# Kernel optimization log

Measured on AMD Instinct MI355X. Metric: run time of the kernel, lower is better.

The kernel has to match this reference:

```python
import jax, jax.numpy as jnp
import numpy as np

EMBED_DIM = 1024
NUM_HEADS = 16
HEAD_DIM = EMBED_DIM // NUM_HEADS
SCALING = HEAD_DIM ** -0.5
NEG_FILL = -1e30


def setup_inputs() -> dict:
    key = jax.random.key(0)
    k1, k2, k3 = jax.random.split(key, 3)
    T, B, E = 2048, 4, EMBED_DIM
    query = jax.random.normal(k1, (T, B, E), dtype=jnp.float32)
    key_padding_mask = jnp.zeros((B, T), dtype=bool)  # 1 = padded key
    # xavier_uniform-like init
    lim_in = (6.0 / (3 * E + E)) ** 0.5
    in_proj_weight = jax.random.uniform(k2, (3 * E, E), minval=-lim_in, maxval=lim_in, dtype=jnp.float32)
    in_proj_bias = jnp.zeros((3 * E,), dtype=jnp.float32)
    lim_out = (6.0 / (E + E)) ** 0.5
    out_w = jax.random.uniform(k3, (E, E), minval=-lim_out, maxval=lim_out, dtype=jnp.float32)
    out_b = jnp.zeros((E,), dtype=jnp.float32)
    return {"query": query, "key_padding_mask": key_padding_mask,
            "in_proj_weight": in_proj_weight, "in_proj_bias": in_proj_bias,
            "out_w": out_w, "out_b": out_b}


def reference(query, key_padding_mask, in_proj_weight, in_proj_bias, out_w, out_b):
    T, B, E = query.shape
    H, D = NUM_HEADS, HEAD_DIM
    # fused in-projection (self-attention: qkv from same input)
    qkv = query @ in_proj_weight.T + in_proj_bias  # [T,B,3E]
    q, k, v = jnp.split(qkv, 3, axis=-1)
    q = q * SCALING
    q = q.reshape(T, B, H, D)
    k = k.reshape(T, B, H, D)
    v = v.reshape(T, B, H, D)
    # attention scores [B,H,T,S]
    scores = jnp.einsum('tbhd,sbhd->bhts', q, k)
    scores = jnp.where(key_padding_mask[:, None, None, :], NEG_FILL, scores)
    attn_w = jax.nn.softmax(scores, axis=-1)  # [B,H,T,S]
    # weighted sum of values -> [T,B,E]
    attn = jnp.einsum('bhts,sbhd->tbhd', attn_w, v).reshape(T, B, E)
    attn = attn @ out_w.T + out_b
    attn_w_avg = jnp.sum(attn_w, axis=1) / H  # [B,T,S]
    return attn, attn_w_avg
```

## Files before the change

### kernel.cpp

```cpp
#include <hip/hip_runtime.h>
#include <stdint.h>

#define QSCALE 0.18033688011112042f

typedef unsigned short u16;
typedef unsigned int u32;
typedef unsigned long long u64;
typedef _Float16 f16;
typedef __attribute__((ext_vector_type(2))) __fp16 h16x2;
typedef __attribute__((ext_vector_type(8))) _Float16 f16x8;
typedef __attribute__((ext_vector_type(8))) __bf16 bf16x8;
typedef __attribute__((ext_vector_type(4))) float f32x4;
typedef __attribute__((ext_vector_type(16))) float f32x16;
typedef __attribute__((ext_vector_type(8))) u16 u16x8;
typedef __attribute__((ext_vector_type(4))) u32 u32x4;

__device__ __forceinline__ void gl_lds16(const void* g, void* l) {
  __builtin_amdgcn_global_load_lds(
      (const __attribute__((address_space(1))) void*)g,
      (__attribute__((address_space(3))) void*)l, 16, 0, 0);
}

__device__ __forceinline__ u16 f2bf(float f) {
  unsigned int u = __float_as_uint(f);
  u += 0x7FFFu + ((u >> 16) & 1u);
  return (u16)(u >> 16);
}

extern "C" __global__ __launch_bounds__(256) void cvt_all(
    const float* __restrict__ query, const float* __restrict__ w_in,
    const float* __restrict__ w_out, u16* __restrict__ dst) {
  int i = (blockIdx.x * 256 + threadIdx.x) * 4;
  const float* src;
  int off;
  if (i < 8388608) {
    src = query; off = i;
  } else if (i < 11534336) {
    src = w_in; off = i - 8388608;
  } else {
    src = w_out; off = i - 11534336;
  }
  float4 v = *(const float4*)(src + off);
  ushort4 o;
  o.x = f2bf(v.x); o.y = f2bf(v.y); o.z = f2bf(v.z); o.w = f2bf(v.w);
  *(ushort4*)(dst + i) = o;
}

extern "C" __global__ __launch_bounds__(128) void mask_bits(
    const unsigned char* __restrict__ mask, u64* __restrict__ mbits) {
  const int i = threadIdx.x;
  const unsigned char* p = mask + i * 64;
  u64 bits = 0;
#pragma unroll
  for (int j = 0; j < 8; ++j) {
    const u64 c = *(const u64*)(p + j * 8);
#pragma unroll
    for (int bb = 0; bb < 8; ++bb)
      if ((c >> (8 * bb)) & 0xFFull) bits |= 1ull << (j * 8 + bb);
  }
  mbits[i] = bits;
}

extern "C" __global__ __launch_bounds__(256) void gemm_qkv(
    const u16* __restrict__ X, const u16* __restrict__ W,
    const float* __restrict__ bias,
    u16* __restrict__ qb, u16* __restrict__ kb, u16* __restrict__ vtb) {
  const int tid = threadIdx.x;
  const int w = tid >> 6, lane = tid & 63;
  const int lg = lane >> 4, ll = lane & 15;
  const int wm = w >> 1, wn = w & 1;

  const int xcd = blockIdx.x & 7;
  const int i6 = blockIdx.x >> 3;
  const int tx = xcd * 8 + (i6 & 7);
  const int ty = i6 >> 3;
  const int row0A = tx * 128;
  const int row0B = ty * 128;

  __shared__ __align__(16) u16 SM[16384];
  u16* Asb = SM;
  u16* Bsb = SM + 8192;

  f32x4 acc[4][4] = {};

  const int r_st = tid >> 2;
  const int cb_st = (tid & 3) * 16;

#pragma unroll
  for (int it = 0; it < 2; ++it) {
    gl_lds16((const char*)X + ((size_t)(row0A + it * 64 + r_st) * 1024) * 2 + cb_st,
             (char*)Asb + it * 4096 + w * 1024);
    gl_lds16((const char*)W + ((size_t)(row0B + it * 64 + r_st) * 1024) * 2 + cb_st,
             (char*)Bsb + it * 4096 + w * 1024);
  }

  for (int kt = 0; kt < 32; ++kt) {
    const int cur = kt & 1;
    asm volatile("s_waitcnt vmcnt(0)" ::: "memory");
    __syncthreads();
    if (kt + 1 < 32) {
      const int k0 = (kt + 1) * 32;
      const int nxt = cur ^ 1;
#pragma unroll
      for (int it = 0; it < 2; ++it) {
        gl_lds16((const char*)X + ((size_t)(row0A + it * 64 + r_st) * 1024 + k0) * 2 + cb_st,
                 (char*)(Asb + nxt * 4096) + it * 4096 + w * 1024);
        gl_lds16((const char*)W + ((size_t)(row0B + it * 64 + r_st) * 1024 + k0) * 2 + cb_st,
                 (char*)(Bsb + nxt * 4096) + it * 4096 + w * 1024);
      }
    }
    const u16* Ab = Asb + cur * 4096;
    const u16* Bb = Bsb + cur * 4096;
    const int kc = lg * 8;
    bf16x8 a[4], bfr[4];
#pragma unroll
    for (int i = 0; i < 4; ++i)
      a[i] = *(const bf16x8*)(Ab + (wm * 64 + i * 16 + ll) * 32 + kc);
#pragma unroll
    for (int j = 0; j < 4; ++j)
      bfr[j] = *(const bf16x8*)(Bb + (wn * 64 + j * 16 + ll) * 32 + kc);
#pragma unroll
    for (int i = 0; i < 4; ++i)
#pragma unroll
      for (int j = 0; j < 4; ++j)
        acc[i][j] = __builtin_amdgcn_mfma_f32_16x16x32_bf16(a[i], bfr[j], acc[i][j], 0, 0, 0);
  }

  __syncthreads();
  const int which = row0B >> 10;
  const float scl = which == 0 ? QSCALE : 1.0f;
  const int hh0 = (row0B & 1023) >> 6;

#pragma unroll
  for (int j = 0; j < 4; ++j) {
    const int n = row0B + wn * 64 + j * 16 + ll;
    const float bv = bias[n];
#pragma unroll
    for (int i = 0; i < 4; ++i)
#pragma unroll
      for (int r = 0; r < 4; ++r) {
        const float val = (acc[i][j][r] + bv) * scl;
        u16 pay;
        if (which == 2) {
          const f16 hv = (f16)val;
          pay = __builtin_bit_cast(u16, hv);
        } else {
          pay = f2bf(val);
        }
        const int lrow = wn * 128 + r * 32 + wm * 16 + i * 4 + lg;
        const int slot = (j * 2 + (ll >> 3)) ^ (lrow & 7);
        SM[lrow * 64 + slot * 8 + (ll & 7)] = pay;
      }
  }
  __syncthreads();

  if (which < 2) {
    u16* dst = which ? kb : qb;
    const int lrow = tid;
    const int hh = hh0 + (lrow >> 7);
    const int bb = (lrow >> 5) & 3;
    const int tt = (row0A >> 2) + (lrow & 31);
    u16* gp = dst + ((size_t)(bb * 16 + hh) * 2048 + tt) * 64;
#pragma unroll
    for (int s = 0; s < 8; ++s)
      *(u16x8*)(gp + s * 8) = *(const u16x8*)(SM + lrow * 64 + ((s ^ (lrow & 7)) << 3));
  } else {
#pragma unroll
    for (int u = 0; u < 2; ++u) {
      const int rid = u * 256 + tid;
      const int bb = rid >> 7, hhr = (rid >> 6) & 1, dd = rid & 63;
      const int hh = hh0 + hhr;
      const int slot0 = dd >> 3, de = dd & 7;
      u16 col[32];
#pragma unroll
      for (int t2 = 0; t2 < 32; ++t2) {
        const int lrow = hhr * 128 + bb * 32 + t2;
        col[t2] = SM[lrow * 64 + ((slot0 ^ (lrow & 7)) << 3) + de];
      }
      u16* gp = vtb + ((size_t)(bb * 16 + hh) * 64 + dd) * 2048 + (row0A >> 2);
#pragma unroll
      for (int sg = 0; sg < 4; ++sg)
        *(u16x8*)(gp + sg * 8) = *(const u16x8*)(col + sg * 8);
    }
  }
}

extern "C" __global__ __launch_bounds__(256, 4) void flash_fwd(
    const u16* __restrict__ q, const u16* __restrict__ k,
    const u16* __restrict__ vt, const u64* __restrict__ mbits,
    u16* __restrict__ attn_pre, float* __restrict__ stat_il) {
  const int lb = ((blockIdx.x & 7) << 7) + (blockIdx.x >> 3);
  const int bh = lb >> 4, tt = lb & 15;
  const int b = bh >> 4, hd = bh & 15;
  const int t0 = tt * 128;
  const int tid = threadIdx.x, w = tid >> 6, lane = tid & 63;
  const int hl = lane >> 5;
  const int l31 = lane & 31;

  __shared__ __align__(16) u16 Ks[2][64 * 64];
  __shared__ __align__(16) u16 Vs[2][64 * 64];

  const int qrow = t0 + w * 32 + l31;
  const u16* qp = q + ((size_t)bh * 2048 + qrow) * 64 + hl * 8;
  bf16x8 qreg[4];
#pragma unroll
  for (int kg = 0; kg < 4; ++kg) qreg[kg] = *(const bf16x8*)(qp + kg * 16);

  f32x16 po[2] = {};
  float ls0 = 0.f, ls1 = 0.f;
  const h16x2 ones = {(__fp16)1.0f, (__fp16)1.0f};

  const int slot_r = tid >> 3;
  const int slot_c8 = (tid & 7) ^ (slot_r & 7);

#define STAGE_F(buf, s0_)                                                      \
  do {                                                                         \
    _Pragma("unroll") for (int it2 = 0; it2 < 2; ++it2) {                      \
      const int rr = it2 * 32 + slot_r;                                        \
      gl_lds16((const char*)k +                                                \
                   (((size_t)bh * 2048 + (s0_) + rr) * 64 + slot_c8 * 8) * 2,  \
               (char*)&Ks[buf][0] + it2 * 4096 + w * 1024);                    \
      gl_lds16((const char*)vt +                                               \
                   (((size_t)bh * 64 + rr) * 2048 + (s0_) + slot_c8 * 8) * 2,  \
               (char*)&Vs[buf][0] + it2 * 4096 + w * 1024);                    \
    }                                                                          \
  } while (0)

  STAGE_F(0, 0);
  asm volatile("s_waitcnt vmcnt(0)" ::: "memory");
  __builtin_amdgcn_s_barrier();

  for (int t = 0; t < 32; ++t) {
    const u64 mb = mbits[b * 32 + t];
    const int cur = t & 1;
    if (t + 1 < 32) STAGE_F(cur ^ 1, (t + 1) * 64);

    const char* Kb = (const char*)&Ks[cur][0];
    const char* Vb = (const char*)&Vs[cur][0];

#pragma unroll
    for (int kt = 0; kt < 2; ++kt) {
      f32x16 z = {};
      const int key = kt * 32 + l31;
      __builtin_amdgcn_s_setprio(1);
#pragma unroll
      for (int kg = 0; kg < 4; ++kg) {
        const bf16x8 kf = *(const bf16x8*)(
            Kb + key * 128 + ((((kg << 1) | hl) ^ (key & 7)) << 4));
        z = __builtin_amdgcn_mfma_f32_32x32x16_bf16(kf, qreg[kg], z, 0, 0, 0);
      }
      __builtin_amdgcn_s_setprio(0);

      float ps[16];
#pragma unroll
      for (int r = 0; r < 16; ++r) ps[r] = __builtin_amdgcn_exp2f(z[r]);
      const u32 m32 = (u32)(mb >> (kt * 32));
      if (m32) {
#pragma unroll
        for (int r = 0; r < 16; ++r) {
          const int bitpos = (r & 3) + 8 * (r >> 2) + 4 * hl;
          if ((m32 >> bitpos) & 1u) ps[r] = 0.f;
        }
      }

      u32 w8[8];
#pragma unroll
      for (int j = 0; j < 8; ++j) {
        const h16x2 pk = __builtin_amdgcn_cvt_pkrtz(ps[2 * j], ps[2 * j + 1]);
        w8[j] = __builtin_bit_cast(u32, pk);
        if (j & 1)
          ls1 = __builtin_amdgcn_fdot2(pk, ones, ls1, false);
        else
          ls0 = __builtin_amdgcn_fdot2(pk, ones, ls0, false);
      }

#pragma unroll
      for (int f = 0; f < 2; ++f) {
        u32 d0 = w8[4 * f], d1 = w8[4 * f + 1];
        u32 s0w = w8[4 * f + 2], s1w = w8[4 * f + 3];
        asm volatile("v_permlane32_swap_b32 %0, %1" : "+v"(d0), "+v"(s0w));
        asm volatile("v_permlane32_swap_b32 %0, %1" : "+v"(d1), "+v"(s1w));
        const f16x8 pa = __builtin_bit_cast(f16x8, (u32x4){d0, d1, s0w, s1w});
        const int g = kt * 2 + f;
        __builtin_amdgcn_s_setprio(1);
#pragma unroll
        for (int dt = 0; dt < 2; ++dt) {
          const int d = dt * 32 + l31;
          const f16x8 vf = *(const f16x8*)(
              Vb + d * 128 + ((((g << 1) | hl) ^ (d & 7)) << 4));
          po[dt] = __builtin_amdgcn_mfma_f32_32x32x16_f16(pa, vf, po[dt], 0, 0, 0);
        }
        __builtin_amdgcn_s_setprio(0);
      }
    }

    asm volatile("s_waitcnt vmcnt(0)" ::: "memory");
    __builtin_amdgcn_s_barrier();
  }

  float lsum = ls0 + ls1;
  lsum += __shfl_xor(lsum, 32, 64);
  const float linv = 1.0f / lsum;
  if (lane < 32)
    stat_il[(size_t)bh * 2048 + t0 + w * 32 + lane] = linv;

#pragma unroll
  for (int r = 0; r < 16; ++r) {
    const int qi = (r & 3) + 8 * (r >> 2) + 4 * hl;
    const float lv = __shfl(linv, qi, 64);
    const int trow = t0 + w * 32 + qi;
#pragma unroll
    for (int dt = 0; dt < 2; ++dt) {
      const int dd = dt * 32 + l31;
      attn_pre[((size_t)(trow * 4 + b)) * 1024 + hd * 64 + dd] =
          f2bf(po[dt][r] * lv);
    }
  }
#undef STAGE_F
}

extern "C" __global__ __launch_bounds__(256, 3) void wavg(
    const u16* __restrict__ q, const u16* __restrict__ k,
    const u64* __restrict__ mbits,
    const float* __restrict__ stat_il, float* __restrict__ wout) {
  const int lb = ((blockIdx.x & 7) << 8) + (blockIdx.x >> 3);
  const int b = lb >> 9, tt = (lb >> 5) & 15, st = lb & 31;
  const int t0 = tt * 128, s0 = st * 64;
  const int tid = threadIdx.x, w = tid >> 6, lane = tid & 63;
  const int hl = lane >> 5;
  const int l31 = lane & 31;

  __shared__ __align__(16) u16 Qs[2][128 * 64];
  __shared__ __align__(16) u16 Ks2[2][64 * 64];

  const int slot_r8 = tid >> 3;
  const int slot_c8 = (tid & 7) ^ (slot_r8 & 7);

  const u64 mbw = mbits[b * 32 + st];
  const u32 m32lo = (u32)mbw, m32hi = (u32)(mbw >> 32);
  const bool domask = mbw != 0ull;

#define STAGE_W(buf, hh)                                                       \
  do {                                                                         \
    const size_t qo_ = (size_t)(b * 16 + (hh)) * 2048;                         \
    _Pragma("unroll") for (int i2 = 0; i2 < 4; ++i2) {                         \
      const int rr = i2 * 32 + slot_r8;                                        \
      gl_lds16((const char*)q + ((qo_ + t0 + rr) * 64 + slot_c8 * 8) * 2,      \
               (char*)&Qs[buf][0] + i2 * 4096 + w * 1024);                     \
    }                                                                          \
    _Pragma("unroll") for (int i2 = 0; i2 < 2; ++i2) {                         \
      const int rr = i2 * 32 + slot_r8;                                        \
      gl_lds16((const char*)k + ((qo_ + s0 + rr) * 64 + slot_c8 * 8) * 2,      \
               (char*)&Ks2[buf][0] + i2 * 4096 + w * 1024);                    \
    }                                                                          \
  } while (0)

  STAGE_W(0, 0);
  asm volatile("s_waitcnt vmcnt(0)" ::: "memory");
  __syncthreads();

  float accw[32] = {};
  for (int h = 0; h < 16; ++h) {
    const int cur = h & 1;
    const float ilh =
        stat_il[(size_t)(b * 16 + h) * 2048 + t0 + w * 32 + l31];

    if (h + 1 < 16) STAGE_W(cur ^ 1, h + 1);

    const char* Qb = (const char*)&Qs[cur][0];
    const char* Kb = (const char*)&Ks2[cur][0];

    const int qr = w * 32 + l31;
    bf16x8 qf[4];
#pragma unroll
    for (int kg = 0; kg < 4; ++kg)
      qf[kg] = *(const bf16x8*)(
          Qb + qr * 128 + ((((kg << 1) | hl) ^ (qr & 7)) << 4));

    f32x16 z0 = {}, z1 = {};
    __builtin_amdgcn_s_setprio(1);
#pragma unroll
    for (int kg = 0; kg < 4; ++kg) {
      const int key = l31;
      const bf16x8 kf = *(const bf16x8*)(
          Kb + key * 128 + ((((kg << 1) | hl) ^ (key & 7)) << 4));
      z0 = __builtin_amdgcn_mfma_f32_32x32x16_bf16(kf, qf[kg], z0, 0, 0, 0);
    }
#pragma unroll
    for (int kg = 0; kg < 4; ++kg) {
      const int key = 32 + l31;
      const bf16x8 kf = *(const bf16x8*)(
          Kb + key * 128 + ((((kg << 1) | hl) ^ (key & 7)) << 4));
      z1 = __builtin_amdgcn_mfma_f32_32x32x16_bf16(kf, qf[kg], z1, 0, 0, 0);
    }
    __builtin_amdgcn_s_setprio(0);

#pragma unroll
    for (int r = 0; r < 16; ++r) {
      float p = __builtin_amdgcn_exp2f(z0[r]);
      if (domask) {
        const int bitpos = (r & 3) + 8 * (r >> 2) + 4 * hl;
        if ((m32lo >> bitpos) & 1u) p = 0.f;
      }
      accw[r] = fmaf(p, ilh, accw[r]);
    }
#pragma unroll
    for (int r = 0; r < 16; ++r) {
      float p = __builtin_amdgcn_exp2f(z1[r]);
      if (domask) {
        const int bitpos = (r & 3) + 8 * (r >> 2) + 4 * hl;
        if ((m32hi >> bitpos) & 1u) p = 0.f;
      }
      accw[16 + r] = fmaf(p, ilh, accw[16 + r]);
    }

    asm volatile("s_waitcnt vmcnt(0)" ::: "memory");
    __syncthreads();
  }

  float* tb = ((float*)&Qs[0][0]) + w * 2048;
#pragma unroll
  for (int kt = 0; kt < 2; ++kt)
#pragma unroll
    for (int j = 0; j < 4; ++j) {
      f32x4 qd;
#pragma unroll
      for (int e = 0; e < 4; ++e) qd[e] = accw[kt * 16 + 4 * j + e] * 0.0625f;
      const int slot = kt * 8 + 2 * j + hl;
      *(f32x4*)(tb + l31 * 64 + ((slot ^ (l31 & 7)) << 2)) = qd;
    }
  __syncthreads();
#pragma unroll
  for (int j2 = 0; j2 < 8; ++j2) {
    const int row = j2 * 4 + (lane >> 4);
    const int slot = lane & 15;
    const f32x4 v = *(const f32x4*)(tb + row * 64 + ((slot ^ (row & 7)) << 2));
    *(f32x4*)(wout + ((size_t)b * 2048 + t0 + w * 32 + row) * 2048 + s0 +
              slot * 4) = v;
  }
#undef STAGE_W
}

extern "C" __global__ __launch_bounds__(256) void gemm_out(
    const u16* __restrict__ A, const u16* __restrict__ W,
    const float* __restrict__ bias, float* __restrict__ out) {
  const int tid = threadIdx.x;
  const int w = tid >> 6, lane = tid & 63;
  const int lg = lane >> 4, ll = lane & 15;
  const int wm = w >> 1, wn = w & 1;

  const int xcd = blockIdx.x & 7;
  const int i6 = blockIdx.x >> 3;
  const int row0A = (xcd * 8 + (i6 & 7)) * 128;
  const int row0B = (i6 >> 3) * 128;

  __shared__ __align__(16) u16 As[2][128 * 32];
  __shared__ __align__(16) u16 Bs[2][128 * 32];

  f32x4 acc[4][4] = {};
  const int r_st = tid >> 2;
  const int cb_st = (tid & 3) * 16;

#pragma unroll
  for (int it = 0; it < 2; ++it) {
    gl_lds16((const char*)A + ((size_t)(row0A + it * 64 + r_st) * 1024) * 2 + cb_st,
             (char*)&As[0][0] + it * 4096 + w * 1024);
    gl_lds16((const char*)W + ((size_t)(row0B + it * 64 + r_st) * 1024) * 2 + cb_st,
             (char*)&Bs[0][0] + it * 4096 + w * 1024);
  }

  for (int kt = 0; kt < 32; ++kt) {
    const int cur = kt & 1;
    asm volatile("s_waitcnt vmcnt(0)" ::: "memory");
    __syncthreads();
    if (kt + 1 < 32) {
      const int k0 = (kt + 1) * 32;
#pragma unroll
      for (int it = 0; it < 2; ++it) {
        gl_lds16((const char*)A + ((size_t)(row0A + it * 64 + r_st) * 1024 + k0) * 2 + cb_st,
                 (char*)&As[cur ^ 1][0] + it * 4096 + w * 1024);
        gl_lds16((const char*)W + ((size_t)(row0B + it * 64 + r_st) * 1024 + k0) * 2 + cb_st,
                 (char*)&Bs[cur ^ 1][0] + it * 4096 + w * 1024);
      }
    }
    const u16* Ab = &As[cur][0];
    const u16* Bb = &Bs[cur][0];
    const int kc = lg * 8;
    bf16x8 a[4], bfr[4];
#pragma unroll
    for (int i = 0; i < 4; ++i)
      a[i] = *(const bf16x8*)(Ab + (wm * 64 + i * 16 + ll) * 32 + kc);
#pragma unroll
    for (int j = 0; j < 4; ++j)
      bfr[j] = *(const bf16x8*)(Bb + (wn * 64 + j * 16 + ll) * 32 + kc);
#pragma unroll
    for (int i = 0; i < 4; ++i)
#pragma unroll
      for (int j = 0; j < 4; ++j)
        acc[i][j] = __builtin_amdgcn_mfma_f32_16x16x32_bf16(a[i], bfr[j], acc[i][j], 0, 0, 0);
  }

#pragma unroll
  for (int j = 0; j < 4; ++j) {
    const int n = row0B + wn * 64 + j * 16 + ll;
    const float bv = bias[n];
#pragma unroll
    for (int i = 0; i < 4; ++i)
#pragma unroll
      for (int r = 0; r < 4; ++r) {
        const int m = row0A + wm * 64 + i * 16 + lg * 4 + r;
        out[(size_t)m * 1024 + n] = acc[i][j][r] + bv;
      }
  }
}

extern "C" void kernel_launch(void* const* d_in, const int* in_sizes, int n_in,
                              void* d_out, int out_size, void* d_ws, size_t ws_size,
                              hipStream_t stream) {
  const float* query = (const float*)d_in[0];
  const unsigned char* mask = (const unsigned char*)d_in[1];
  const float* w_in = (const float*)d_in[2];
  const float* b_in = (const float*)d_in[3];
  const float* w_out = (const float*)d_in[4];
  const float* b_out = (const float*)d_in[5];

  float* out0 = (float*)d_out;
  float* outw = out0 + (size_t)8388608;

  char* ws = (char*)d_ws;
  u16* Xbf   = (u16*)(ws + 0);
  u16* Wqkv  = (u16*)(ws + 16777216);
  u16* Woutb = (u16*)(ws + 23068672);
  u16* qb    = (u16*)(ws + 25165824);
  u16* kb    = (u16*)(ws + 41943040);
  u16* vtb   = (u16*)(ws + 75497472);
  u16* ap    = (u16*)(ws + 92274688);
  float* sil = (float*)(ws + 109051904);
  u64* mbits = (u64*)(ws + 109576192);

  cvt_all<<<12288, 256, 0, stream>>>(query, w_in, w_out, Xbf);
  mask_bits<<<1, 128, 0, stream>>>(mask, mbits);
  gemm_qkv<<<1536, 256, 0, stream>>>(Xbf, Wqkv, b_in, qb, kb, vtb);
  flash_fwd<<<1024, 256, 0, stream>>>(qb, kb, vtb, mbits, ap, sil);
  wavg<<<2048, 256, 0, stream>>>(qb, kb, mbits, sil, outw);
  gemm_out<<<512, 256, 0, stream>>>(ap, Woutb, b_out, out0);
}
```

Before: 280.1 us.

## Merge mask packing into convert kernel and co-schedule wavg with out-projection GEMM

The mask bit-packing work moves into an extra block of the conversion kernel, which removes one kernel launch. The head-averaged attention-weight kernel and the output-projection GEMM are combined into one launch. Blocks are interleaved so that every fifth block runs a GEMM tile and the other four run wavg tiles, with both sharing one LDS pool. This removes a launch and the tail gap between the two kernels and lets the GEMM overlap the memory-bound wavg. In exchange, the larger shared LDS allocation applies to the GEMM blocks too, which may reduce their occupancy.

```diff
diff --git a/kernel.cpp b/kernel.cpp
--- a/kernel.cpp
+++ b/kernel.cpp
@@ -29,7 +29,24 @@
 
 extern "C" __global__ __launch_bounds__(256) void cvt_all(
     const float* __restrict__ query, const float* __restrict__ w_in,
-    const float* __restrict__ w_out, u16* __restrict__ dst) {
+    const float* __restrict__ w_out, u16* __restrict__ dst,
+    const unsigned char* __restrict__ mask, u64* __restrict__ mbits) {
+  if (blockIdx.x == 12288) {
+    const int i = threadIdx.x;
+    if (i < 128) {
+      const unsigned char* p = mask + i * 64;
+      u64 bits = 0;
+#pragma unroll
+      for (int j = 0; j < 8; ++j) {
+        const u64 c = *(const u64*)(p + j * 8);
+#pragma unroll
+        for (int bb = 0; bb < 8; ++bb)
+          if ((c >> (8 * bb)) & 0xFFull) bits |= 1ull << (j * 8 + bb);
+      }
+      mbits[i] = bits;
+    }
+    return;
+  }
   int i = (blockIdx.x * 256 + threadIdx.x) * 4;
   const float* src;
   int off;
@@ -44,21 +61,6 @@
   ushort4 o;
   o.x = f2bf(v.x); o.y = f2bf(v.y); o.z = f2bf(v.z); o.w = f2bf(v.w);
   *(ushort4*)(dst + i) = o;
-}
-
-extern "C" __global__ __launch_bounds__(128) void mask_bits(
-    const unsigned char* __restrict__ mask, u64* __restrict__ mbits) {
-  const int i = threadIdx.x;
-  const unsigned char* p = mask + i * 64;
-  u64 bits = 0;
-#pragma unroll
-  for (int j = 0; j < 8; ++j) {
-    const u64 c = *(const u64*)(p + j * 8);
-#pragma unroll
-    for (int bb = 0; bb < 8; ++bb)
-      if ((c >> (8 * bb)) & 0xFFull) bits |= 1ull << (j * 8 + bb);
-  }
-  mbits[i] = bits;
 }
 
 extern "C" __global__ __launch_bounds__(256) void gemm_qkv(
@@ -319,19 +321,93 @@
 #undef STAGE_F
 }
 
-extern "C" __global__ __launch_bounds__(256, 3) void wavg(
+extern "C" __global__ __launch_bounds__(256, 3) void tail_fused(
     const u16* __restrict__ q, const u16* __restrict__ k,
-    const u64* __restrict__ mbits,
-    const float* __restrict__ stat_il, float* __restrict__ wout) {
-  const int lb = ((blockIdx.x & 7) << 8) + (blockIdx.x >> 3);
+    const u64* __restrict__ mbits, const float* __restrict__ stat_il,
+    float* __restrict__ wout,
+    const u16* __restrict__ A, const u16* __restrict__ Wo,
+    const float* __restrict__ bias, float* __restrict__ out) {
+  __shared__ __align__(16) u16 POOL[24576];
+  const int bid = blockIdx.x;
+  const int g5 = bid / 5, r5 = bid % 5;
+  const int tid = threadIdx.x, w = tid >> 6, lane = tid & 63;
+
+  if (r5 == 4) {
+    const int lg = lane >> 4, ll = lane & 15;
+    const int wm = w >> 1, wn = w & 1;
+    const int xcd = g5 & 7;
+    const int i6 = g5 >> 3;
+    const int row0A = (xcd * 8 + (i6 & 7)) * 128;
+    const int row0B = (i6 >> 3) * 128;
+
+    u16* Asb = POOL;
+    u16* Bsb = POOL + 8192;
+
+    f32x4 acc[4][4] = {};
+    const int r_st = tid >> 2;
+    const int cb_st = (tid & 3) * 16;
+
+#pragma unroll
+    for (int it = 0; it < 2; ++it) {
+      gl_lds16((const char*)A + ((size_t)(row0A + it * 64 + r_st) * 1024) * 2 + cb_st,
+               (char*)Asb + it * 4096 + w * 1024);
+      gl_lds16((const char*)Wo + ((size_t)(row0B + it * 64 + r_st) * 1024) * 2 + cb_st,
+               (char*)Bsb + it * 4096 + w * 1024);
+    }
+
+    for (int kt = 0; kt < 32; ++kt) {
+      const int cur = kt & 1;
+      asm volatile("s_waitcnt vmcnt(0)" ::: "memory");
+      __syncthreads();
+      if (kt + 1 < 32) {
+        const int k0 = (kt + 1) * 32;
+        const int nxt = cur ^ 1;
+#pragma unroll
+        for (int it = 0; it < 2; ++it) {
+          gl_lds16((const char*)A + ((size_t)(row0A + it * 64 + r_st) * 1024 + k0) * 2 + cb_st,
+                   (char*)(Asb + nxt * 4096) + it * 4096 + w * 1024);
+          gl_lds16((const char*)Wo + ((size_t)(row0B + it * 64 + r_st) * 1024 + k0) * 2 + cb_st,
+                   (char*)(Bsb + nxt * 4096) + it * 4096 + w * 1024);
+        }
+      }
+      const u16* Ab = Asb + cur * 4096;
+      const u16* Bb = Bsb + cur * 4096;
+      const int kc = lg * 8;
+      bf16x8 a[4], bfr[4];
+#pragma unroll
+      for (int i = 0; i < 4; ++i)
+        a[i] = *(const bf16x8*)(Ab + (wm * 64 + i * 16 + ll) * 32 + kc);
+#pragma unroll
+      for (int j = 0; j < 4; ++j)
+        bfr[j] = *(const bf16x8*)(Bb + (wn * 64 + j * 16 + ll) * 32 + kc);
+#pragma unroll
+      for (int i = 0; i < 4; ++i)
+#pragma unroll
+        for (int j = 0; j < 4; ++j)
+          acc[i][j] = __builtin_amdgcn_mfma_f32_16x16x32_bf16(a[i], bfr[j], acc[i][j], 0, 0, 0);
+    }
+
+#pragma unroll
+    for (int j = 0; j < 4; ++j) {
+      const int n = row0B + wn * 64 + j * 16 + ll;
+      const float bv = bias[n];
+#pragma unroll
+      for (int i = 0; i < 4; ++i)
+#pragma unroll
+        for (int r = 0; r < 4; ++r) {
+          const int m = row0A + wm * 64 + i * 16 + lg * 4 + r;
+          out[(size_t)m * 1024 + n] = acc[i][j][r] + bv;
+        }
+    }
+    return;
+  }
+
+  const int wb = g5 * 4 + r5;
+  const int lb = ((wb & 7) << 8) + (wb >> 3);
   const int b = lb >> 9, tt = (lb >> 5) & 15, st = lb & 31;
   const int t0 = tt * 128, s0 = st * 64;
-  const int tid = threadIdx.x, w = tid >> 6, lane = tid & 63;
   const int hl = lane >> 5;
   const int l31 = lane & 31;
-
-  __shared__ __align__(16) u16 Qs[2][128 * 64];
-  __shared__ __align__(16) u16 Ks2[2][64 * 64];
 
   const int slot_r8 = tid >> 3;
   const int slot_c8 = (tid & 7) ^ (slot_r8 & 7);
@@ -346,12 +422,12 @@
     _Pragma("unroll") for (int i2 = 0; i2 < 4; ++i2) {                         \
       const int rr = i2 * 32 + slot_r8;                                        \
       gl_lds16((const char*)q + ((qo_ + t0 + rr) * 64 + slot_c8 * 8) * 2,      \
-               (char*)&Qs[buf][0] + i2 * 4096 + w * 1024);                     \
+               (char*)(POOL + (buf)*8192) + i2 * 4096 + w * 1024);             \
     }                                                                          \
     _Pragma("unroll") for (int i2 = 0; i2 < 2; ++i2) {                         \
       const int rr = i2 * 32 + slot_r8;                                        \
       gl_lds16((const char*)k + ((qo_ + s0 + rr) * 64 + slot_c8 * 8) * 2,      \
-               (char*)&Ks2[buf][0] + i2 * 4096 + w * 1024);                    \
+               (char*)(POOL + 16384 + (buf)*4096) + i2 * 4096 + w * 1024);     \
     }                                                                          \
   } while (0)
 
@@ -367,8 +443,8 @@
 
     if (h + 1 < 16) STAGE_W(cur ^ 1, h + 1);
 
-    const char* Qb = (const char*)&Qs[cur][0];
-    const char* Kb = (const char*)&Ks2[cur][0];
+    const char* Qb = (const char*)(POOL + cur * 8192);
+    const char* Kb = (const char*)(POOL + 16384 + cur * 4096);
 
     const int qr = w * 32 + l31;
     bf16x8 qf[4];
@@ -418,7 +494,7 @@
     __syncthreads();
   }
 
-  float* tb = ((float*)&Qs[0][0]) + w * 2048;
+  float* tb = ((float*)POOL) + w * 2048;
 #pragma unroll
   for (int kt = 0; kt < 2; ++kt)
 #pragma unroll
@@ -439,79 +515,6 @@
               slot * 4) = v;
   }
 #undef STAGE_W
-}
-
-extern "C" __global__ __launch_bounds__(256) void gemm_out(
-    const u16* __restrict__ A, const u16* __restrict__ W,
-    const float* __restrict__ bias, float* __restrict__ out) {
-  const int tid = threadIdx.x;
-  const int w = tid >> 6, lane = tid & 63;
-  const int lg = lane >> 4, ll = lane & 15;
-  const int wm = w >> 1, wn = w & 1;
-
-  const int xcd = blockIdx.x & 7;
-  const int i6 = blockIdx.x >> 3;
-  const int row0A = (xcd * 8 + (i6 & 7)) * 128;
-  const int row0B = (i6 >> 3) * 128;
-
-  __shared__ __align__(16) u16 As[2][128 * 32];
-  __shared__ __align__(16) u16 Bs[2][128 * 32];
-
-  f32x4 acc[4][4] = {};
-  const int r_st = tid >> 2;
-  const int cb_st = (tid & 3) * 16;
-
-#pragma unroll
-  for (int it = 0; it < 2; ++it) {
-    gl_lds16((const char*)A + ((size_t)(row0A + it * 64 + r_st) * 1024) * 2 + cb_st,
-             (char*)&As[0][0] + it * 4096 + w * 1024);
-    gl_lds16((const char*)W + ((size_t)(row0B + it * 64 + r_st) * 1024) * 2 + cb_st,
-             (char*)&Bs[0][0] + it * 4096 + w * 1024);
-  }
-
-  for (int kt = 0; kt < 32; ++kt) {
-    const int cur = kt & 1;
-    asm volatile("s_waitcnt vmcnt(0)" ::: "memory");
-    __syncthreads();
-    if (kt + 1 < 32) {
-      const int k0 = (kt + 1) * 32;
-#pragma unroll
-      for (int it = 0; it < 2; ++it) {
-        gl_lds16((const char*)A + ((size_t)(row0A + it * 64 + r_st) * 1024 + k0) * 2 + cb_st,
-                 (char*)&As[cur ^ 1][0] + it * 4096 + w * 1024);
-        gl_lds16((const char*)W + ((size_t)(row0B + it * 64 + r_st) * 1024 + k0) * 2 + cb_st,
-                 (char*)&Bs[cur ^ 1][0] + it * 4096 + w * 1024);
-      }
-    }
-    const u16* Ab = &As[cur][0];
-    const u16* Bb = &Bs[cur][0];
-    const int kc = lg * 8;
-    bf16x8 a[4], bfr[4];
-#pragma unroll
-    for (int i = 0; i < 4; ++i)
-      a[i] = *(const bf16x8*)(Ab + (wm * 64 + i * 16 + ll) * 32 + kc);
-#pragma unroll
-    for (int j = 0; j < 4; ++j)
-      bfr[j] = *(const bf16x8*)(Bb + (wn * 64 + j * 16 + ll) * 32 + kc);
-#pragma unroll
-    for (int i = 0; i < 4; ++i)
-#pragma unroll
-      for (int j = 0; j < 4; ++j)
-        acc[i][j] = __builtin_amdgcn_mfma_f32_16x16x32_bf16(a[i], bfr[j], acc[i][j], 0, 0, 0);
-  }
-
-#pragma unroll
-  for (int j = 0; j < 4; ++j) {
-    const int n = row0B + wn * 64 + j * 16 + ll;
-    const float bv = bias[n];
-#pragma unroll
-    for (int i = 0; i < 4; ++i)
-#pragma unroll
-      for (int r = 0; r < 4; ++r) {
-        const int m = row0A + wm * 64 + i * 16 + lg * 4 + r;
-        out[(size_t)m * 1024 + n] = acc[i][j][r] + bv;
-      }
-  }
 }
 
 extern "C" void kernel_launch(void* const* d_in, const int* in_sizes, int n_in,
@@ -538,10 +541,9 @@
   float* sil = (float*)(ws + 109051904);
   u64* mbits = (u64*)(ws + 109576192);
 
-  cvt_all<<<12288, 256, 0, stream>>>(query, w_in, w_out, Xbf);
-  mask_bits<<<1, 128, 0, stream>>>(mask, mbits);
+  cvt_all<<<12289, 256, 0, stream>>>(query, w_in, w_out, Xbf, mask, mbits);
   gemm_qkv<<<1536, 256, 0, stream>>>(Xbf, Wqkv, b_in, qb, kb, vtb);
   flash_fwd<<<1024, 256, 0, stream>>>(qb, kb, vtb, mbits, ap, sil);
-  wavg<<<2048, 256, 0, stream>>>(qb, kb, mbits, sil, outw);
-  gemm_out<<<512, 256, 0, stream>>>(ap, Woutb, b_out, out0);
-}
+  tail_fused<<<2560, 256, 0, stream>>>(qb, kb, mbits, sil, outw,
+                                       ap, Woutb, b_out, out0);
+}
```

After: 269.5 us, median of 2. 1.04x faster.
